# Optimization experiments

Hardware: AMD Instinct MI355X
Metric: run time of the kernel (lower is better)

## Reference

```python
import jax, jax.numpy as jnp
import numpy as np

MAX_SH_DEGREE = 3
NUM_BASES = (MAX_SH_DEGREE + 1) ** 2  # 16


def eval_sh_bases_fast(dirs):
    """SH bases up to degree 3 for unit directions [..., 3] -> [..., 16].
    Matches gsplat's _eval_sh_bases_fast constants/order."""
    x, y, z = dirs[..., 0], dirs[..., 1], dirs[..., 2]
    z2 = z * z
    fTmp0B = -1.092548430592079 * z
    fC1 = x * x - y * y
    fS1 = 2.0 * x * y
    fTmp0C = -2.285228997322329 * z2 + 0.4570457994644658
    fTmp1B = 1.445305721320277 * z
    fC2 = x * fC1 - y * fS1
    fS2 = x * fS1 + y * fC1
    ones = jnp.full_like(x, 0.2820947917738781)
    return jnp.stack([
        ones,
        -0.48860251190292 * y,
        0.48860251190292 * z,
        -0.48860251190292 * x,
        0.5462742152960395 * fS1,
        fTmp0B * y,
        0.9461746957575601 * z2 - 0.3153915652525201,
        fTmp0B * x,
        0.5462742152960395 * fC1,
        -0.5900435899266435 * fS2,
        fTmp1B * fS1,
        fTmp0C * y,
        z * (1.865881662950577 * z2 - 1.119528997770346),
        fTmp0C * x,
        fTmp1B * fC1,
        -0.5900435899266435 * fC2,
    ], axis=-1)


def setup_inputs() -> dict:
    key = jax.random.key(0)
    ks = jax.random.split(key, 10)
    C, N, F, E, W = 4, 250000, 32, 16, 128
    D_IN = E + F + NUM_BASES  # 64
    return {
        "features": jax.random.normal(ks[0], (N, F), jnp.float32),
        "dirs": jax.random.normal(ks[1], (C, N, 3), jnp.float32),
        "embed_table": jax.random.normal(ks[2], (1000, E), jnp.float32) * 0.1,
        "W0": jax.random.normal(ks[3], (D_IN, W), jnp.float32) / np.sqrt(D_IN),
        "b0": jax.random.normal(ks[4], (W,), jnp.float32) * 0.01,
        "W1": jax.random.normal(ks[5], (W, W), jnp.float32) / np.sqrt(W),
        "b1": jax.random.normal(ks[6], (W,), jnp.float32) * 0.01,
        "W2": jax.random.normal(ks[7], (W, 3), jnp.float32) / np.sqrt(W),
        "b2": jax.random.normal(ks[8], (3,), jnp.float32) * 0.01,
        "embed_ids": jax.random.randint(ks[9], (C,), 0, 1000, jnp.int64 if jax.config.jax_enable_x64 else jnp.int32),
        "sh_degree": 3,
    }


def reference(features, dirs, embed_table, W0, b0, W1, b1, W2, b2, embed_ids, sh_degree):
    C, N = dirs.shape[:2]
    E = embed_table.shape[1]
    F_dim = features.shape[1]
    # camera embeddings broadcast over splats
    emb = embed_table[embed_ids]                                   # [C, E]
    emb = jnp.broadcast_to(emb[:, None, :], (C, N, E))
    feats = jnp.broadcast_to(features[None, :, :], (C, N, F_dim))
    # F.normalize(dirs, dim=-1): divide by norm clamped at eps=1e-12
    norm = jnp.linalg.norm(dirs, axis=-1, keepdims=True)
    nd = dirs / jnp.maximum(norm, 1e-12)
    nb_use = (sh_degree + 1) ** 2  # static python int
    sh = eval_sh_bases_fast(nd)                                    # [C, N, 16]
    if nb_use < NUM_BASES:  # zero bases beyond requested degree
        mask = (jnp.arange(NUM_BASES) < nb_use).astype(sh.dtype)
        sh = sh * mask
    x = jnp.concatenate([emb, feats, sh], axis=-1)                 # [C, N, 64]
    h = jax.nn.relu(x @ W0 + b0)
    h = jax.nn.relu(h @ W1 + b1)
    return h @ W2 + b2                                             # [C, N, 3]
```

## Files before the change

### kernel.cpp

```cpp
#include <hip/hip_runtime.h>
#include <cstdint>
#include <cstddef>

typedef _Float16 half8 __attribute__((ext_vector_type(8)));
typedef __fp16 fp16x2 __attribute__((ext_vector_type(2)));
typedef float floatx16 __attribute__((ext_vector_type(16)));
typedef unsigned uint2v __attribute__((ext_vector_type(2)));


__global__ void vdc_prep_kernel(const float* __restrict__ W0,
                                const float* __restrict__ W1,
                                const float* __restrict__ W2,
                                const float* __restrict__ b0,
                                const float* __restrict__ b1,
                                const float* __restrict__ b2,
                                const float* __restrict__ emb_tab,
                                const int* __restrict__ embed_ids,
                                int C,
                                _Float16* __restrict__ ws) {
    int i = blockIdx.x * 256 + threadIdx.x;
    int w0end = C * 8192;
    int w1end = w0end + 18432;
    int w2end = w1end + 4608;
    float v = 0.0f;
    if (i < w0end) {
        int c = i >> 13, r = i & 8191;
        int ci = r >> 9, l = (r >> 3) & 63, ii = r & 7;
        int mt = ci >> 2, ks = ci & 3;
        int j  = mt * 32 + (l & 31);
        int kk = ks * 16 + (l >> 5) * 8 + ii;
        if (kk < 48) v = W0[(16 + kk) * 128 + j];
        else if (kk == 48) {
            int id = embed_ids[c];
            v = b0[j];
            #pragma unroll
            for (int e = 0; e < 16; ++e)
                v += emb_tab[(size_t)id * 16 + e] * W0[e * 128 + j];
        }
        ws[i] = (_Float16)v;
    } else if (i < w1end) {
        int r = i - w0end;
        int ci = r >> 9, l = (r >> 3) & 63, ii = r & 7;
        int mt = ci / 9, ks = ci - mt * 9;
        int j  = mt * 32 + (l & 31);
        int kk = ks * 16 + (l >> 5) * 8 + ii;
        if (kk < 128) v = W1[kk * 128 + j];
        else if (kk == 128) v = b1[j];
        ws[i] = (_Float16)v;
    } else if (i < w2end) {
        int r = i - w1end;
        int ks = r >> 9, l = (r >> 3) & 63, ii = r & 7;
        int o  = l & 31;
        int kk = ks * 16 + (l >> 5) * 8 + ii;
        if (o < 3) {
            if (kk < 128) v = W2[kk * 3 + o];
            else if (kk == 128) v = b2[o];
        }
        ws[i] = (_Float16)v;
    }
}

union U4 { unsigned u[4]; half8 h; };

__device__ __forceinline__ unsigned pkr(float a, float b) {
    union { fp16x2 h; unsigned u; } x;
    x.h = __builtin_amdgcn_cvt_pkrtz(a, b);
    return x.u;
}

__device__ __forceinline__ unsigned pkrelu(float a, float b) {
    union { fp16x2 h; unsigned u; } x;
    x.h = __builtin_amdgcn_cvt_pkrtz(a, b);
    fp16x2 z = {(__fp16)0.0f, (__fp16)0.0f};
    x.h = __builtin_elementwise_max(x.h, z);
    return x.u;
}

__device__ __forceinline__ floatx16 zero16() {
    floatx16 z;
    #pragma unroll
    for (int r = 0; r < 16; ++r) z[r] = 0.0f;
    return z;
}

__device__ __forceinline__ void transition(const floatx16& a, int hl,
                                           half8& lo, half8& hi) {
    unsigned p0 = pkrelu(a[0],  a[1]);
    unsigned p1 = pkrelu(a[2],  a[3]);
    unsigned p2 = pkrelu(a[4],  a[5]);
    unsigned p3 = pkrelu(a[6],  a[7]);
    unsigned p4 = pkrelu(a[8],  a[9]);
    unsigned p5 = pkrelu(a[10], a[11]);
    unsigned p6 = pkrelu(a[12], a[13]);
    unsigned p7 = pkrelu(a[14], a[15]);
    U4 L, H;
#if __has_builtin(__builtin_amdgcn_permlane32_swap)
    uint2v s02 = __builtin_amdgcn_permlane32_swap(p0, p2, false, false);
    uint2v s13 = __builtin_amdgcn_permlane32_swap(p1, p3, false, false);
    uint2v s46 = __builtin_amdgcn_permlane32_swap(p4, p6, false, false);
    uint2v s57 = __builtin_amdgcn_permlane32_swap(p5, p7, false, false);
    L.u[0] = s02[0]; L.u[1] = s13[0]; L.u[2] = s02[1]; L.u[3] = s13[1];
    H.u[0] = s46[0]; H.u[1] = s57[0]; H.u[2] = s46[1]; H.u[3] = s57[1];
    (void)hl;
#else
    unsigned r0 = __shfl_xor(hl ? p0 : p2, 32);
    unsigned r1 = __shfl_xor(hl ? p1 : p3, 32);
    unsigned r2 = __shfl_xor(hl ? p4 : p6, 32);
    unsigned r3 = __shfl_xor(hl ? p5 : p7, 32);
    L.u[0] = hl ? r0 : p0;
    L.u[1] = hl ? r1 : p1;
    L.u[2] = hl ? p2 : r0;
    L.u[3] = hl ? p3 : r1;
    H.u[0] = hl ? r2 : p4;
    H.u[1] = hl ? r3 : p5;
    H.u[2] = hl ? p6 : r2;
    H.u[3] = hl ? p7 : r3;
#endif
    lo = L.h; hi = H.h;
}

__device__ __forceinline__ void build_bfrags(
    const float* __restrict__ feats, const float* __restrict__ dirs,
    size_t cN, int n, int hl, int nbu,
    half8& o0, half8& o1, half8& o2)
{
    const float* fp = feats + (size_t)n * 32 + hl * 8;
    float4 f0 = *(const float4*)(fp);
    float4 f1 = *(const float4*)(fp + 4);
    float4 f2 = *(const float4*)(fp + 16);
    float4 f3 = *(const float4*)(fp + 20);
    U4 u0, u1;
    u0.u[0] = pkr(f0.x, f0.y); u0.u[1] = pkr(f0.z, f0.w);
    u0.u[2] = pkr(f1.x, f1.y); u0.u[3] = pkr(f1.z, f1.w);
    u1.u[0] = pkr(f2.x, f2.y); u1.u[1] = pkr(f2.z, f2.w);
    u1.u[2] = pkr(f3.x, f3.y); u1.u[3] = pkr(f3.z, f3.w);
    o0 = u0.h; o1 = u1.h;

    const float* dp = dirs + (cN + n) * 3;
    float dx = dp[0], dy = dp[1], dz = dp[2];
    float nrm = sqrtf(dx * dx + dy * dy + dz * dz);
    float inv = 1.0f / fmaxf(nrm, 1e-12f);
    float x = dx * inv, y = dy * inv, z = dz * inv;

    float z2     = z * z;
    float fTmp0B = -1.092548430592079f * z;
    float fC1    = x * x - y * y;
    float fS1    = 2.0f * x * y;
    float fTmp0C = -2.285228997322329f * z2 + 0.4570457994644658f;
    float fTmp1B = 1.445305721320277f * z;
    float fC2    = x * fC1 - y * fS1;
    float fS2    = x * fS1 + y * fC1;

    float sh[16];
    sh[0]  = 0.2820947917738781f;
    sh[1]  = -0.48860251190292f * y;
    sh[2]  = 0.48860251190292f * z;
    sh[3]  = -0.48860251190292f * x;
    sh[4]  = 0.5462742152960395f * fS1;
    sh[5]  = fTmp0B * y;
    sh[6]  = 0.9461746957575601f * z2 - 0.3153915652525201f;
    sh[7]  = fTmp0B * x;
    sh[8]  = 0.5462742152960395f * fC1;
    sh[9]  = -0.5900435899266435f * fS2;
    sh[10] = fTmp1B * fS1;
    sh[11] = fTmp0C * y;
    sh[12] = z * (1.865881662950577f * z2 - 1.119528997770346f);
    sh[13] = fTmp0C * x;
    sh[14] = fTmp1B * fC1;
    sh[15] = -0.5900435899266435f * fC2;
    #pragma unroll
    for (int i = 0; i < 16; ++i) if (i >= nbu) sh[i] = 0.0f;

    float s0 = hl ? sh[8]  : sh[0];
    float s1 = hl ? sh[9]  : sh[1];
    float s2 = hl ? sh[10] : sh[2];
    float s3 = hl ? sh[11] : sh[3];
    float s4 = hl ? sh[12] : sh[4];
    float s5 = hl ? sh[13] : sh[5];
    float s6 = hl ? sh[14] : sh[6];
    float s7 = hl ? sh[15] : sh[7];
    U4 u2;
    u2.u[0] = pkr(s0, s1); u2.u[1] = pkr(s2, s3);
    u2.u[2] = pkr(s4, s5); u2.u[3] = pkr(s6, s7);
    o2 = u2.h;
}

#define MFMA(a, b, c) __builtin_amdgcn_mfma_f32_32x32x16_f16((a), (b), (c), 0, 0, 0)
#define LDF(off) (*(const half8*)(fr + (off)))
#define GW2(ch) (*(const half8*)(w2p + (ch) * 512 + lane * 8))

#define L0_MT(MT, HA0, HA1, HB0, HB1)                                    \
    do {                                                                 \
        floatx16 ca = zero16();                                          \
        floatx16 cb = zero16();                                          \
        half8 t0 = LDF(((MT) * 4 + 0) * 1024);                           \
        ca = MFMA(t0, ax0, ca); cb = MFMA(t0, bx0, cb);                  \
        half8 t1 = LDF(((MT) * 4 + 1) * 1024);                           \
        ca = MFMA(t1, ax1, ca); cb = MFMA(t1, bx1, cb);                  \
        half8 t2 = LDF(((MT) * 4 + 2) * 1024);                           \
        ca = MFMA(t2, ax2, ca); cb = MFMA(t2, bx2, cb);                  \
        half8 t3 = LDF(((MT) * 4 + 3) * 1024);                           \
        ca = MFMA(t3, bbias, ca); cb = MFMA(t3, bbias, cb);              \
        transition(ca, hl, HA0, HA1);                                    \
        transition(cb, hl, HB0, HB1);                                    \
    } while (0)

#define L1_KS(MT, KS, HA, HB)                                            \
    do {                                                                 \
        half8 q = LDF(16384 + ((MT) * 9 + (KS)) * 1024);                 \
        ca = MFMA(q, HA, ca); cb = MFMA(q, HB, cb);                      \
    } while (0)

#define L1_MT(MT)                                                        \
    do {                                                                 \
        floatx16 ca = zero16();                                          \
        floatx16 cb = zero16();                                          \
        L1_KS(MT, 0, ha0, hb0);                                          \
        L1_KS(MT, 1, ha1, hb1);                                          \
        L1_KS(MT, 2, ha2, hb2);                                          \
        L1_KS(MT, 3, ha3, hb3);                                          \
        L1_KS(MT, 4, ha4, hb4);                                          \
        L1_KS(MT, 5, ha5, hb5);                                          \
        L1_KS(MT, 6, ha6, hb6);                                          \
        L1_KS(MT, 7, ha7, hb7);                                          \
        L1_KS(MT, 8, bbias, bbias);                                      \
        half8 w2a = GW2(2 * (MT) + 0);                                   \
        half8 w2b = GW2(2 * (MT) + 1);                                   \
        half8 g0, g1;                                                    \
        transition(ca, hl, g0, g1);                                      \
        acc3a = MFMA(w2a, g0, acc3a); acc3a = MFMA(w2b, g1, acc3a);      \
        transition(cb, hl, g0, g1);                                      \
        acc3b = MFMA(w2a, g0, acc3b); acc3b = MFMA(w2b, g1, acc3b);      \
    } while (0)

__global__ __launch_bounds__(256, 3) void vdc_mlp_kernel(
    const float* __restrict__ feats,
    const float* __restrict__ dirs,
    const int* __restrict__ sh_deg_p,
    const _Float16* __restrict__ ws,
    float* __restrict__ out,
    int N, int C)
{
    __shared__ uint4 arena[3328];
    char* lds = (char*)arena;

    const int tid   = threadIdx.x;
    const int c     = blockIdx.y;
    const int w     = tid >> 6;
    const int lane  = tid & 63;
    const int ln    = lane & 31;
    const int hl    = lane >> 5;
    const int base  = blockIdx.x * 256 + w * 64;

    const _Float16* w2p = ws + (size_t)C * 8192 + 18432;

    {
        const uint4* srcA = (const uint4*)(ws + (size_t)c * 8192);
        const uint4* srcB = (const uint4*)(ws + (size_t)C * 8192);
        #pragma unroll
        for (int it = 0; it < 13; ++it) {
            int idx = it * 256 + tid;
            arena[idx] = (idx < 1024) ? srcA[idx] : srcB[idx - 1024];
        }
    }

    half8 bbias;
    {
        U4 ub;
        ub.u[0] = hl ? 0u : 0x00003C00u;
        ub.u[1] = 0u; ub.u[2] = 0u; ub.u[3] = 0u;
        bbias = ub.h;
    }
    int deg = sh_deg_p[0];
    int nbu = (deg + 1) * (deg + 1);
    int na = base + ln;      if (na >= N) na = N - 1;
    int nb = base + 32 + ln; if (nb >= N) nb = N - 1;
    half8 ax0, ax1, ax2, bx0, bx1, bx2;
    build_bfrags(feats, dirs, (size_t)c * N, na, hl, nbu, ax0, ax1, ax2);
    build_bfrags(feats, dirs, (size_t)c * N, nb, hl, nbu, bx0, bx1, bx2);

    __syncthreads();

    const char* fr = lds + lane * 16;

    half8 ha0, ha1, ha2, ha3, ha4, ha5, ha6, ha7;
    half8 hb0, hb1, hb2, hb3, hb4, hb5, hb6, hb7;
    L0_MT(0, ha0, ha1, hb0, hb1);
    L0_MT(1, ha2, ha3, hb2, hb3);
    L0_MT(2, ha4, ha5, hb4, hb5);
    L0_MT(3, ha6, ha7, hb6, hb7);

    floatx16 acc3a = zero16();
    floatx16 acc3b = zero16();
    L1_MT(0);
    L1_MT(1);
    L1_MT(2);
    L1_MT(3);
    {
        half8 ab = GW2(8);
        acc3a = MFMA(ab, bbias, acc3a);
        acc3b = MFMA(ab, bbias, acc3b);
    }

    if (hl == 0) {
        int nn = base + ln;
        if (nn < N) {
            float* op = out + ((size_t)c * N + nn) * 3;
            op[0] = acc3a[0];
            op[1] = acc3a[1];
            op[2] = acc3a[2];
        }
        nn = base + 32 + ln;
        if (nn < N) {
            float* op = out + ((size_t)c * N + nn) * 3;
            op[0] = acc3b[0];
            op[1] = acc3b[1];
            op[2] = acc3b[2];
        }
    }
}

extern "C" void kernel_launch(void* const* d_in, const int* in_sizes, int n_in,
                              void* d_out, int out_size, void* d_ws, size_t ws_size,
                              hipStream_t stream) {
    const float* feats   = (const float*)d_in[0];
    const float* dirs    = (const float*)d_in[1];
    const float* emb_tab = (const float*)d_in[2];
    const float* W0      = (const float*)d_in[3];
    const float* b0      = (const float*)d_in[4];
    const float* W1      = (const float*)d_in[5];
    const float* b1      = (const float*)d_in[6];
    const float* W2      = (const float*)d_in[7];
    const float* b2      = (const float*)d_in[8];
    const int*   eids    = (const int*)d_in[9];
    const int*   shd     = (const int*)d_in[10];
    float* outp          = (float*)d_out;

    int N = in_sizes[0] / 32;
    int C = in_sizes[9];

    _Float16* wsh = (_Float16*)d_ws;

    int ws_elems = C * 8192 + 23040;
    vdc_prep_kernel<<<(ws_elems + 255) / 256, 256, 0, stream>>>(
        W0, W1, W2, b0, b1, b2, emb_tab, eids, C, wsh);

    dim3 grid((N + 255) / 256, C);
    vdc_mlp_kernel<<<grid, 256, 0, stream>>>(
        feats, dirs, shd, wsh, outp, N, C);
}
```

Before: 146.9 us.

## Loop each block over two chunks to amortize weight staging, restructure final layer

```diff
diff --git a/kernel.cpp b/kernel.cpp
--- a/kernel.cpp
+++ b/kernel.cpp
@@ -76,13 +76,6 @@
     return x.u;
 }
 
-__device__ __forceinline__ floatx16 zero16() {
-    floatx16 z;
-    #pragma unroll
-    for (int r = 0; r < 16; ++r) z[r] = 0.0f;
-    return z;
-}
-
 __device__ __forceinline__ void transition(const floatx16& a, int hl,
                                            half8& lo, half8& hi) {
     unsigned p0 = pkrelu(a[0],  a[1]);
@@ -119,25 +112,8 @@
     lo = L.h; hi = H.h;
 }
 
-__device__ __forceinline__ void build_bfrags(
-    const float* __restrict__ feats, const float* __restrict__ dirs,
-    size_t cN, int n, int hl, int nbu,
-    half8& o0, half8& o1, half8& o2)
-{
-    const float* fp = feats + (size_t)n * 32 + hl * 8;
-    float4 f0 = *(const float4*)(fp);
-    float4 f1 = *(const float4*)(fp + 4);
-    float4 f2 = *(const float4*)(fp + 16);
-    float4 f3 = *(const float4*)(fp + 20);
-    U4 u0, u1;
-    u0.u[0] = pkr(f0.x, f0.y); u0.u[1] = pkr(f0.z, f0.w);
-    u0.u[2] = pkr(f1.x, f1.y); u0.u[3] = pkr(f1.z, f1.w);
-    u1.u[0] = pkr(f2.x, f2.y); u1.u[1] = pkr(f2.z, f2.w);
-    u1.u[2] = pkr(f3.x, f3.y); u1.u[3] = pkr(f3.z, f3.w);
-    o0 = u0.h; o1 = u1.h;
-
-    const float* dp = dirs + (cN + n) * 3;
-    float dx = dp[0], dy = dp[1], dz = dp[2];
+__device__ __forceinline__ void sh_frag(float dx, float dy, float dz,
+                                        int hl, int nbu, half8& o2) {
     float nrm = sqrtf(dx * dx + dy * dy + dz * dz);
     float inv = 1.0f / fmaxf(nrm, 1e-12f);
     float x = dx * inv, y = dy * inv, z = dz * inv;
@@ -185,21 +161,59 @@
     o2 = u2.h;
 }
 
+__device__ __forceinline__ void build_bfrags2(
+    const float* __restrict__ feats, const float* __restrict__ dirs,
+    size_t cN, int na, int nb, int hl, int nbu,
+    half8& ao0, half8& ao1, half8& ao2,
+    half8& bo0, half8& bo1, half8& bo2)
+{
+    const float* fa = feats + (size_t)na * 32 + hl * 8;
+    const float* fb = feats + (size_t)nb * 32 + hl * 8;
+    float4 fa0 = *(const float4*)(fa);
+    float4 fa1 = *(const float4*)(fa + 4);
+    float4 fa2 = *(const float4*)(fa + 16);
+    float4 fa3 = *(const float4*)(fa + 20);
+    float4 fb0 = *(const float4*)(fb);
+    float4 fb1 = *(const float4*)(fb + 4);
+    float4 fb2 = *(const float4*)(fb + 16);
+    float4 fb3 = *(const float4*)(fb + 20);
+    const float* dpa = dirs + (cN + na) * 3;
+    const float* dpb = dirs + (cN + nb) * 3;
+    float dax = dpa[0], day = dpa[1], daz = dpa[2];
+    float dbx = dpb[0], dby = dpb[1], dbz = dpb[2];
+
+    U4 u;
+    u.u[0] = pkr(fa0.x, fa0.y); u.u[1] = pkr(fa0.z, fa0.w);
+    u.u[2] = pkr(fa1.x, fa1.y); u.u[3] = pkr(fa1.z, fa1.w);
+    ao0 = u.h;
+    u.u[0] = pkr(fa2.x, fa2.y); u.u[1] = pkr(fa2.z, fa2.w);
+    u.u[2] = pkr(fa3.x, fa3.y); u.u[3] = pkr(fa3.z, fa3.w);
+    ao1 = u.h;
+    u.u[0] = pkr(fb0.x, fb0.y); u.u[1] = pkr(fb0.z, fb0.w);
+    u.u[2] = pkr(fb1.x, fb1.y); u.u[3] = pkr(fb1.z, fb1.w);
+    bo0 = u.h;
+    u.u[0] = pkr(fb2.x, fb2.y); u.u[1] = pkr(fb2.z, fb2.w);
+    u.u[2] = pkr(fb3.x, fb3.y); u.u[3] = pkr(fb3.z, fb3.w);
+    bo1 = u.h;
+
+    sh_frag(dax, day, daz, hl, nbu, ao2);
+    sh_frag(dbx, dby, dbz, hl, nbu, bo2);
+}
+
 #define MFMA(a, b, c) __builtin_amdgcn_mfma_f32_32x32x16_f16((a), (b), (c), 0, 0, 0)
 #define LDF(off) (*(const half8*)(fr + (off)))
 #define GW2(ch) (*(const half8*)(w2p + (ch) * 512 + lane * 8))
 
 #define L0_MT(MT, HA0, HA1, HB0, HB1)                                    \
     do {                                                                 \
-        floatx16 ca = zero16();                                          \
-        floatx16 cb = zero16();                                          \
         half8 t0 = LDF(((MT) * 4 + 0) * 1024);                           \
-        ca = MFMA(t0, ax0, ca); cb = MFMA(t0, bx0, cb);                  \
         half8 t1 = LDF(((MT) * 4 + 1) * 1024);                           \
+        half8 t2 = LDF(((MT) * 4 + 2) * 1024);                           \
+        half8 t3 = LDF(((MT) * 4 + 3) * 1024);                           \
+        floatx16 ca = MFMA(t0, ax0, z);                                  \
+        floatx16 cb = MFMA(t0, bx0, z);                                  \
         ca = MFMA(t1, ax1, ca); cb = MFMA(t1, bx1, cb);                  \
-        half8 t2 = LDF(((MT) * 4 + 2) * 1024);                           \
         ca = MFMA(t2, ax2, ca); cb = MFMA(t2, bx2, cb);                  \
-        half8 t3 = LDF(((MT) * 4 + 3) * 1024);                           \
         ca = MFMA(t3, bbias, ca); cb = MFMA(t3, bbias, cb);              \
         transition(ca, hl, HA0, HA1);                                    \
         transition(cb, hl, HB0, HB1);                                    \
@@ -211,11 +225,14 @@
         ca = MFMA(q, HA, ca); cb = MFMA(q, HB, cb);                      \
     } while (0)
 
-#define L1_MT(MT)                                                        \
+#define PFW2(M) w2a##M = GW2(2 * (M)); w2b##M = GW2(2 * (M) + 1)
+
+#define L1_MT(MT, W2A, W2B, PF)                                          \
     do {                                                                 \
-        floatx16 ca = zero16();                                          \
-        floatx16 cb = zero16();                                          \
-        L1_KS(MT, 0, ha0, hb0);                                          \
+        floatx16 ca, cb;                                                 \
+        { half8 q = LDF(16384 + ((MT) * 9 + 0) * 1024);                  \
+          ca = MFMA(q, ha0, z); cb = MFMA(q, hb0, z); }                  \
+        PF;                                                              \
         L1_KS(MT, 1, ha1, hb1);                                          \
         L1_KS(MT, 2, ha2, hb2);                                          \
         L1_KS(MT, 3, ha3, hb3);                                          \
@@ -224,13 +241,13 @@
         L1_KS(MT, 6, ha6, hb6);                                          \
         L1_KS(MT, 7, ha7, hb7);                                          \
         L1_KS(MT, 8, bbias, bbias);                                      \
-        half8 w2a = GW2(2 * (MT) + 0);                                   \
-        half8 w2b = GW2(2 * (MT) + 1);                                   \
         half8 g0, g1;                                                    \
         transition(ca, hl, g0, g1);                                      \
-        acc3a = MFMA(w2a, g0, acc3a); acc3a = MFMA(w2b, g1, acc3a);      \
+        { floatx16 ct = MFMA(W2A, g0, z); ct = MFMA(W2B, g1, ct);        \
+          oa0 += ct[0]; oa1 += ct[1]; oa2 += ct[2]; }                    \
         transition(cb, hl, g0, g1);                                      \
-        acc3b = MFMA(w2a, g0, acc3b); acc3b = MFMA(w2b, g1, acc3b);      \
+        { floatx16 ct = MFMA(W2A, g0, z); ct = MFMA(W2B, g1, ct);        \
+          ob0 += ct[0]; ob1 += ct[1]; ob2 += ct[2]; }                    \
     } while (0)
 
 __global__ __launch_bounds__(256, 3) void vdc_mlp_kernel(
@@ -238,8 +255,9 @@
     const float* __restrict__ dirs,
     const int* __restrict__ sh_deg_p,
     const _Float16* __restrict__ ws,
+    const float* __restrict__ b2p,
     float* __restrict__ out,
-    int N, int C)
+    int N, int C, int nchunk)
 {
     __shared__ uint4 arena[3328];
     char* lds = (char*)arena;
@@ -250,7 +268,6 @@
     const int lane  = tid & 63;
     const int ln    = lane & 31;
     const int hl    = lane >> 5;
-    const int base  = blockIdx.x * 256 + w * 64;
 
     const _Float16* w2p = ws + (size_t)C * 8192 + 18432;
 
@@ -273,49 +290,54 @@
     }
     int deg = sh_deg_p[0];
     int nbu = (deg + 1) * (deg + 1);
-    int na = base + ln;      if (na >= N) na = N - 1;
-    int nb = base + 32 + ln; if (nb >= N) nb = N - 1;
-    half8 ax0, ax1, ax2, bx0, bx1, bx2;
-    build_bfrags(feats, dirs, (size_t)c * N, na, hl, nbu, ax0, ax1, ax2);
-    build_bfrags(feats, dirs, (size_t)c * N, nb, hl, nbu, bx0, bx1, bx2);
+    float b20 = b2p[0], b21 = b2p[1], b22 = b2p[2];
+
+    float zf;
+    asm volatile("v_mov_b32 %0, 0" : "=v"(zf));
+    floatx16 z;
+    #pragma unroll
+    for (int r = 0; r < 16; ++r) z[r] = zf;
 
     __syncthreads();
 
     const char* fr = lds + lane * 16;
 
-    half8 ha0, ha1, ha2, ha3, ha4, ha5, ha6, ha7;
-    half8 hb0, hb1, hb2, hb3, hb4, hb5, hb6, hb7;
-    L0_MT(0, ha0, ha1, hb0, hb1);
-    L0_MT(1, ha2, ha3, hb2, hb3);
-    L0_MT(2, ha4, ha5, hb4, hb5);
-    L0_MT(3, ha6, ha7, hb6, hb7);
-
-    floatx16 acc3a = zero16();
-    floatx16 acc3b = zero16();
-    L1_MT(0);
-    L1_MT(1);
-    L1_MT(2);
-    L1_MT(3);
-    {
-        half8 ab = GW2(8);
-        acc3a = MFMA(ab, bbias, acc3a);
-        acc3b = MFMA(ab, bbias, acc3b);
-    }
-
-    if (hl == 0) {
-        int nn = base + ln;
-        if (nn < N) {
-            float* op = out + ((size_t)c * N + nn) * 3;
-            op[0] = acc3a[0];
-            op[1] = acc3a[1];
-            op[2] = acc3a[2];
-        }
-        nn = base + 32 + ln;
-        if (nn < N) {
-            float* op = out + ((size_t)c * N + nn) * 3;
-            op[0] = acc3b[0];
-            op[1] = acc3b[1];
-            op[2] = acc3b[2];
+    for (int chunk = blockIdx.x; chunk < nchunk; chunk += gridDim.x) {
+        const int base = chunk * 256 + w * 64;
+        int na = base + ln;      if (na >= N) na = N - 1;
+        int nb = base + 32 + ln; if (nb >= N) nb = N - 1;
+
+        half8 ax0, ax1, ax2, bx0, bx1, bx2;
+        build_bfrags2(feats, dirs, (size_t)c * N, na, nb, hl, nbu,
+                      ax0, ax1, ax2, bx0, bx1, bx2);
+
+        half8 ha0, ha1, ha2, ha3, ha4, ha5, ha6, ha7;
+        half8 hb0, hb1, hb2, hb3, hb4, hb5, hb6, hb7;
+        half8 w2a0, w2b0, w2a1, w2b1, w2a2, w2b2, w2a3, w2b3;
+        L0_MT(0, ha0, ha1, hb0, hb1);
+        L0_MT(1, ha2, ha3, hb2, hb3);
+        L0_MT(2, ha4, ha5, hb4, hb5);
+        PFW2(0);
+        L0_MT(3, ha6, ha7, hb6, hb7);
+
+        float oa0 = b20, oa1 = b21, oa2 = b22;
+        float ob0 = b20, ob1 = b21, ob2 = b22;
+        L1_MT(0, w2a0, w2b0, PFW2(1));
+        L1_MT(1, w2a1, w2b1, PFW2(2));
+        L1_MT(2, w2a2, w2b2, PFW2(3));
+        L1_MT(3, w2a3, w2b3, );
+
+        if (hl == 0) {
+            int nn = base + ln;
+            if (nn < N) {
+                float* op = out + ((size_t)c * N + nn) * 3;
+                op[0] = oa0; op[1] = oa1; op[2] = oa2;
+            }
+            nn = base + 32 + ln;
+            if (nn < N) {
+                float* op = out + ((size_t)c * N + nn) * 3;
+                op[0] = ob0; op[1] = ob1; op[2] = ob2;
+            }
         }
     }
 }
@@ -345,7 +367,10 @@
     vdc_prep_kernel<<<(ws_elems + 255) / 256, 256, 0, stream>>>(
         W0, W1, W2, b0, b1, b2, emb_tab, eids, C, wsh);
 
-    dim3 grid((N + 255) / 256, C);
+    int nchunk = (N + 255) / 256;
+    int gx = (nchunk + 1) / 2;
+    if (gx < 1) gx = 1;
+    dim3 grid(gx, C);
     vdc_mlp_kernel<<<grid, 256, 0, stream>>>(
-        feats, dirs, shd, wsh, outp, N, C);
-}
+        feats, dirs, shd, wsh, b2, outp, N, C, nchunk);
+}
```

Result: slower. 493.3 us (+235.9%).
